# Performance work log

Measured on AMD Instinct MI355X. Metric: run time of the kernel, lower is better.

The kernel has to match this reference:

```python
import jax, jax.numpy as jnp
import numpy as np

NUM_CLASSES = 10
LAMBDA_COORD = 5.0
LAMBDA_NOOBJ = 0.5
B, S, P = 2048, 26, 5 + NUM_CLASSES


def setup_inputs() -> dict:
    key = jax.random.key(0)
    k1, k2 = jax.random.split(key)
    predictions = jax.random.normal(k1, (B, S, S, P), dtype=jnp.float32)
    targets = jax.random.normal(k2, (B, S * S * P,), dtype=jnp.float32)
    return {"predictions": predictions, "targets": targets}


def reference(predictions, targets):
    b, s, _, p = predictions.shape
    pred = predictions.reshape(b, s * s, p)          # (B, S*S, 5+C)
    tgt = targets.reshape(b, s * s, -1)              # (B, S*S, 5+C)

    obj = tgt[..., 4] > 0                            # object mask per cell

    # Coordinate loss: lambda_coord * sum((pred_xywh - tgt_xywh)^2) over object cells
    coord_sq = jnp.sum((pred[..., :4] - tgt[..., :4]) ** 2, axis=-1)
    coord_loss = LAMBDA_COORD * jnp.sum(jnp.where(obj, coord_sq, 0.0))

    # Confidence loss: (sigmoid(p_conf) - t_conf)^2 on obj cells,
    # lambda_noobj * sigmoid(p_conf)^2 on no-obj cells (scalar MSE mean == squared diff)
    conf_p = jax.nn.sigmoid(pred[..., 4])
    conf_loss = jnp.sum(jnp.where(obj,
                                  (conf_p - tgt[..., 4]) ** 2,
                                  LAMBDA_NOOBJ * conf_p ** 2))

    # Classification loss: mean over C of squared diff per object cell, summed
    cls_sq = jnp.mean((pred[..., 5:5 + NUM_CLASSES] - tgt[..., 5:5 + NUM_CLASSES]) ** 2, axis=-1)
    class_loss = jnp.sum(jnp.where(obj, cls_sq, 0.0))

    total_loss = coord_loss + conf_loss + class_loss
    return (total_loss, coord_loss, conf_loss, class_loss)
```

## Files before the change

### kernel.cpp

```cpp
#include <hip/hip_runtime.h>

constexpr int   NUM_CLASSES  = 10;
constexpr float LAMBDA_COORD = 5.0f;
constexpr float LAMBDA_NOOBJ = 0.5f;
constexpr int   BLOCK = 256;
constexpr int   NBLOCKS_MAX = 2048;

__global__ __launch_bounds__(BLOCK) void yolo_main(
    const float4* __restrict__ pred4,
    const float4* __restrict__ tgt4,
    const float*  __restrict__ tgt,
    float* __restrict__ ws,
    unsigned n4, unsigned nblocks)
{
    unsigned idx    = blockIdx.x * BLOCK + threadIdx.x;
    unsigned stride = nblocks * BLOCK;

    float coord = 0.f, conf = 0.f, cls = 0.f;

    for (unsigned k = idx; k < n4; k += stride) {
        float4 p = pred4[k];
        float4 t = tgt4[k];
        unsigned base  = 4u * k;
        unsigned cell0 = base / 15u;
        unsigned j0    = base - cell0 * 15u;

        float t4a = tgt[cell0 * 15u + 4u];
        float t4b = (j0 >= 12u) ? tgt[cell0 * 15u + 19u] : t4a;

        float pm[4] = {p.x, p.y, p.z, p.w};
        float tm[4] = {t.x, t.y, t.z, t.w};

#pragma unroll
        for (int m = 0; m < 4; ++m) {
            unsigned j      = j0 + (unsigned)m;
            bool     second = j >= 15u;
            unsigned jj     = second ? j - 15u : j;
            float    t4     = second ? t4b : t4a;
            bool     obj    = t4 > 0.f;

            float d  = pm[m] - tm[m];
            float sq = d * d;

            float sig   = 1.f / (1.f + __expf(-pm[m]));
            float dsv   = sig - tm[m];
            float confv = obj ? dsv * dsv : LAMBDA_NOOBJ * sig * sig;

            if (jj < 4u)       { if (obj) coord += sq; }
            else if (jj == 4u) { conf += confv; }
            else               { if (obj) cls += sq; }
        }
    }

#pragma unroll
    for (int off = 32; off > 0; off >>= 1) {
        coord += __shfl_down(coord, off);
        conf  += __shfl_down(conf,  off);
        cls   += __shfl_down(cls,   off);
    }

    __shared__ float s[3][4];
    int wave = threadIdx.x >> 6, lane = threadIdx.x & 63;
    if (lane == 0) { s[0][wave] = coord; s[1][wave] = conf; s[2][wave] = cls; }
    __syncthreads();

    if (threadIdx.x == 0) {
        float c0 = s[0][0] + s[0][1] + s[0][2] + s[0][3];
        float c1 = s[1][0] + s[1][1] + s[1][2] + s[1][3];
        float c2 = s[2][0] + s[2][1] + s[2][2] + s[2][3];
        ws[blockIdx.x]               = c0;
        ws[nblocks + blockIdx.x]     = c1;
        ws[2 * nblocks + blockIdx.x] = c2;
    }
}

__global__ __launch_bounds__(BLOCK) void yolo_finalize(
    const float* __restrict__ ws, float* __restrict__ out, unsigned nblocks)
{
    float c0 = 0.f, c1 = 0.f, c2 = 0.f;
    for (unsigned i = threadIdx.x; i < nblocks; i += BLOCK) {
        c0 += ws[i];
        c1 += ws[nblocks + i];
        c2 += ws[2 * nblocks + i];
    }
#pragma unroll
    for (int off = 32; off > 0; off >>= 1) {
        c0 += __shfl_down(c0, off);
        c1 += __shfl_down(c1, off);
        c2 += __shfl_down(c2, off);
    }
    __shared__ float s[3][4];
    int wave = threadIdx.x >> 6, lane = threadIdx.x & 63;
    if (lane == 0) { s[0][wave] = c0; s[1][wave] = c1; s[2][wave] = c2; }
    __syncthreads();
    if (threadIdx.x == 0) {
        float coord = LAMBDA_COORD * (s[0][0] + s[0][1] + s[0][2] + s[0][3]);
        float conf  =                 s[1][0] + s[1][1] + s[1][2] + s[1][3];
        float cls   = (1.f / NUM_CLASSES) * (s[2][0] + s[2][1] + s[2][2] + s[2][3]);
        out[0] = coord + conf + cls;
        out[1] = coord;
        out[2] = conf;
        out[3] = cls;
    }
}

extern "C" void kernel_launch(void* const* d_in, const int* in_sizes, int n_in,
                              void* d_out, int out_size, void* d_ws, size_t ws_size,
                              hipStream_t stream) {
    const float* pred = (const float*)d_in[0];
    const float* tgt  = (const float*)d_in[1];
    float* out = (float*)d_out;
    float* ws  = (float*)d_ws;

    unsigned total = (unsigned)in_sizes[0];
    unsigned n4    = total / 4u;

    unsigned nblocks = NBLOCKS_MAX;
    size_t need = (size_t)nblocks * 3 * sizeof(float);
    if (need > ws_size) nblocks = (unsigned)(ws_size / (3 * sizeof(float)));

    yolo_main<<<nblocks, BLOCK, 0, stream>>>(
        (const float4*)pred, (const float4*)tgt, tgt, ws, n4, nblocks);
    yolo_finalize<<<1, BLOCK, 0, stream>>>(ws, out, nblocks);
}
```

Baseline: 182.0 us.

## Unroll grid-stride loop by five and compute one sigmoid per float4

The grid-stride loop is unrolled five times so all loads for five iterations are issued before any compute, giving more memory-level parallelism. The per-element logic becomes branchless, and the sigmoid is computed once per float4 on the single confidence element that can fall in it, instead of four times. The block count changes from 2048 to 2028, presumably so the element count divides evenly across the unrolled stride. The extra loads and unrolling raise register pressure.

```diff
diff --git a/kernel.cpp b/kernel.cpp
--- a/kernel.cpp
+++ b/kernel.cpp
@@ -4,7 +4,40 @@
 constexpr float LAMBDA_COORD = 5.0f;
 constexpr float LAMBDA_NOOBJ = 0.5f;
 constexpr int   BLOCK = 256;
-constexpr int   NBLOCKS_MAX = 2048;
+constexpr int   NBLOCKS_MAX = 2028;
+constexpr int   UNROLL = 5;
+
+__device__ __forceinline__ void slot(const float4 p, const float4 t,
+                                     const float t4a, const float t4b,
+                                     unsigned j0,
+                                     float& coord, float& conf, float& cls)
+{
+    const float pm[4] = {p.x, p.y, p.z, p.w};
+    const float tm[4] = {t.x, t.y, t.z, t.w};
+
+#pragma unroll
+    for (int m = 0; m < 4; ++m) {
+        unsigned j  = j0 + (unsigned)m;
+        float d     = pm[m] - tm[m];
+        float sq    = d * d;
+        float t4    = (j >= 15u) ? t4b : t4a;
+        float sqo   = (t4 > 0.f) ? sq : 0.f;
+        coord += ((j - 4u) >= 11u) ? sqo : 0.f;
+        cls   += ((j - 5u) <  10u) ? sqo : 0.f;
+    }
+
+    bool  hasConf = (j0 - 1u) < 4u;
+    float pc = (j0 == 4u) ? pm[0]
+             : (j0 == 3u) ? pm[1]
+             : (j0 == 2u) ? pm[2]
+             :              pm[3];
+    float e   = __expf(-pc);
+    float sig = 1.f / (1.f + e);
+    bool  obj = t4a > 0.f;
+    float dsv = sig - t4a;
+    float confv = obj ? dsv * dsv : LAMBDA_NOOBJ * sig * sig;
+    conf += hasConf ? confv : 0.f;
+}
 
 __global__ __launch_bounds__(BLOCK) void yolo_main(
     const float4* __restrict__ pred4,
@@ -18,38 +51,41 @@
 
     float coord = 0.f, conf = 0.f, cls = 0.f;
 
-    for (unsigned k = idx; k < n4; k += stride) {
+    unsigned k = idx;
+    for (; k + (UNROLL - 1) * stride < n4; k += UNROLL * stride) {
+        float4   p[UNROLL], t[UNROLL];
+        float    ta[UNROLL], tb[UNROLL];
+        unsigned j0s[UNROLL];
+
+#pragma unroll
+        for (int u = 0; u < UNROLL; ++u) {
+            unsigned kk    = k + (unsigned)u * stride;
+            p[u]           = pred4[kk];
+            t[u]           = tgt4[kk];
+            unsigned base  = 4u * kk;
+            unsigned cell0 = base / 15u;
+            unsigned c15   = cell0 * 15u;
+            unsigned j0    = base - c15;
+            j0s[u]         = j0;
+            ta[u]          = tgt[c15 + 4u];
+            tb[u]          = tgt[(j0 >= 12u) ? c15 + 19u : c15 + 4u];
+        }
+
+#pragma unroll
+        for (int u = 0; u < UNROLL; ++u)
+            slot(p[u], t[u], ta[u], tb[u], j0s[u], coord, conf, cls);
+    }
+
+    for (; k < n4; k += stride) {
         float4 p = pred4[k];
         float4 t = tgt4[k];
         unsigned base  = 4u * k;
         unsigned cell0 = base / 15u;
-        unsigned j0    = base - cell0 * 15u;
-
-        float t4a = tgt[cell0 * 15u + 4u];
-        float t4b = (j0 >= 12u) ? tgt[cell0 * 15u + 19u] : t4a;
-
-        float pm[4] = {p.x, p.y, p.z, p.w};
-        float tm[4] = {t.x, t.y, t.z, t.w};
-
-#pragma unroll
-        for (int m = 0; m < 4; ++m) {
-            unsigned j      = j0 + (unsigned)m;
-            bool     second = j >= 15u;
-            unsigned jj     = second ? j - 15u : j;
-            float    t4     = second ? t4b : t4a;
-            bool     obj    = t4 > 0.f;
-
-            float d  = pm[m] - tm[m];
-            float sq = d * d;
-
-            float sig   = 1.f / (1.f + __expf(-pm[m]));
-            float dsv   = sig - tm[m];
-            float confv = obj ? dsv * dsv : LAMBDA_NOOBJ * sig * sig;
-
-            if (jj < 4u)       { if (obj) coord += sq; }
-            else if (jj == 4u) { conf += confv; }
-            else               { if (obj) cls += sq; }
-        }
+        unsigned c15   = cell0 * 15u;
+        unsigned j0    = base - c15;
+        float ta = tgt[c15 + 4u];
+        float tb = tgt[(j0 >= 12u) ? c15 + 19u : c15 + 4u];
+        slot(p, t, ta, tb, j0, coord, conf, cls);
     }
 
 #pragma unroll
```

Result: no change. 185.0 us (+1.7%).
